# Kernel tuning notes

Hardware: AMD Instinct MI355X
Metric: run time of the kernel (lower is better)

Reference implementation:

```python
import jax, jax.numpy as jnp
import numpy as np

N, E, D, L = 10000, 160000, 512, 3
NEG_SLOPE = 0.2
LN_EPS = 1e-5


def setup_inputs() -> dict:
    key = jax.random.key(0)
    ks = jax.random.split(key, 16)
    def rn(k, shape, scale=0.02):
        return jax.random.normal(k, shape, dtype=jnp.float32) * scale
    return {
        "x": jax.random.normal(ks[0], (N, D), dtype=jnp.float32),
        "edge_attr": jax.random.normal(ks[1], (E, 2), dtype=jnp.float32),
        "emb_inv_W": rn(ks[2], (D, D)), "emb_inv_b": jnp.zeros((D,), jnp.float32),
        "emb_org_W": rn(ks[3], (D, D)), "emb_org_b": jnp.zeros((D,), jnp.float32),
        "gat_Wl": rn(ks[4], (L, D, D)), "gat_bl": jnp.zeros((L, D), jnp.float32),
        "gat_Wr": rn(ks[5], (L, D, D)), "gat_br": jnp.zeros((L, D), jnp.float32),
        "gat_We": rn(ks[6], (L, 2, D)),
        "gat_att": rn(ks[7], (L, D), 0.1),
        "gat_bias": jnp.zeros((L, D), jnp.float32),
        "ln_g": jnp.ones((L, D), jnp.float32), "ln_b": jnp.zeros((L, D), jnp.float32),
        "lin0_W": rn(ks[8], (2 * D, D)), "lin0_b": jnp.zeros((D,), jnp.float32),
        "lin1_W": rn(ks[9], (2 * D, D)), "lin1_b": jnp.zeros((D,), jnp.float32),
        "edge_index": jax.random.randint(ks[10], (2, E), 0, N, dtype=jnp.int32),
        "n_inv": 4000,
        "n_unknown": 3000,
    }


def _layernorm(x, g, b):
    m = jnp.mean(x, axis=-1, keepdims=True)
    v = jnp.mean((x - m) ** 2, axis=-1, keepdims=True)
    return (x - m) * jax.lax.rsqrt(v + LN_EPS) * g + b


def _gatv2(x, src, dst, edge_attr, Wl, bl, Wr, br, We, att, bias):
    # single-head GATv2: e_ij = att . leaky_relu(Wl x_j + Wr x_i + We e_ij)
    xl = x @ Wl + bl                                  # [N,D] source transform
    xr = x @ Wr + br                                  # [N,D] target transform
    m = xl[src] + xr[dst] + edge_attr @ We            # [E,D]
    s = jax.nn.leaky_relu(m, NEG_SLOPE) @ att         # [E] attention logits
    smax = jax.ops.segment_max(s, dst, num_segments=N)  # per-target max
    a = jnp.exp(s - smax[dst])
    denom = jax.ops.segment_sum(a, dst, num_segments=N)
    alpha = a / jnp.where(denom[dst] > 0, denom[dst], 1.0)  # [E]
    out = jax.ops.segment_sum(alpha[:, None] * xl[src], dst, num_segments=N)
    return out + bias


def _forward(x, edge_attr, emb_inv_W, emb_inv_b, emb_org_W, emb_org_b,
             gat_Wl, gat_bl, gat_Wr, gat_br, gat_We, gat_att, gat_bias,
             ln_g, ln_b, lin0_W, lin0_b, lin1_W, lin1_b,
             edge_index, n_inv, n_unknown):
    src, dst = edge_index[0], edge_index[1]
    x0 = x[:n_inv] @ emb_inv_W + emb_inv_b           # [n_inv, D]
    x1 = x[n_inv:] @ emb_org_W + emb_org_b           # [N-n_inv, D]
    h = jnp.concatenate([x0, x1], axis=0)            # [N, D]
    for k in range(L):
        hc = _gatv2(h, src, dst, edge_attr,
                    gat_Wl[k], gat_bl[k], gat_Wr[k], gat_br[k],
                    gat_We[k], gat_att[k], gat_bias[k])
        h = jax.nn.relu(_layernorm(hc + h, ln_g[k], ln_b[k]))
    y0 = jnp.concatenate([x0, h[:n_inv]], axis=-1) @ lin0_W + lin0_b          # [n_inv, D]
    y1 = jnp.concatenate([x1[-n_unknown:], h[-n_unknown:]], axis=-1) @ lin1_W + lin1_b  # [n_unknown, D]
    return y0 @ y1.T                                  # [n_inv, n_unknown]


def reference(x, edge_attr, emb_inv_W, emb_inv_b, emb_org_W, emb_org_b,
              gat_Wl, gat_bl, gat_Wr, gat_br, gat_We, gat_att, gat_bias,
              ln_g, ln_b, lin0_W, lin0_b, lin1_W, lin1_b,
              edge_index, n_inv, n_unknown):
    return _forward(x, edge_attr, emb_inv_W, emb_inv_b, emb_org_W, emb_org_b,
                    gat_Wl, gat_bl, gat_Wr, gat_br, gat_We, gat_att, gat_bias,
                    ln_g, ln_b, lin0_W, lin0_b, lin1_W, lin1_b,
                    edge_index, n_inv, n_unknown)
```

## Files before the change

kernel.cpp:

```cpp
#include <hip/hip_runtime.h>
#include <cstddef>
#include <cstdint>

namespace {

using u16 = unsigned short;
typedef __attribute__((ext_vector_type(8))) unsigned short u16x8;
typedef __attribute__((ext_vector_type(8))) short bf16x8;
typedef __attribute__((ext_vector_type(4))) float f32x4;

constexpr int kN    = 10000;
constexpr int kE    = 160000;
constexpr int kD    = 512;
constexpr int kNinv = 4000;
constexpr int kNunk = 3000;
constexpr int kND   = kN * kD;
constexpr float kLnEps = 1e-5f;

__device__ __forceinline__ float bf2f(u16 u) {
  return __uint_as_float((unsigned)u << 16);
}
__device__ __forceinline__ u16 f2bf(float f) {
  unsigned u = __float_as_uint(f);
  return (u16)((u + 0x7FFFu + ((u >> 16) & 1u)) >> 16);
}

__device__ __forceinline__ void gload_lds16(const void* g, void* l) {
  __builtin_amdgcn_global_load_lds(
      (const __attribute__((address_space(1))) void*)(unsigned long long)(uintptr_t)g,
      (__attribute__((address_space(3))) void*)(unsigned)(uintptr_t)l,
      16, 0, 0);
}

template <bool WRITE_F32, bool WRITE_BF16>
__global__ __launch_bounds__(256) void gemm_bf16(
    const u16* __restrict__ A1, const u16* __restrict__ A2,
    const u16* __restrict__ BT, const float* __restrict__ bias,
    float* __restrict__ Cf, u16* __restrict__ Cb, u16* __restrict__ Cb2,
    int nsplit, int M, int N, int K, int ldc) {
  __shared__ u16 As[128 * 64];
  __shared__ u16 Bs[128 * 64];
  const int tid  = threadIdx.x;
  const int lane = tid & 63;
  const int wid  = tid >> 6;

  const int nwg = gridDim.x * gridDim.y;
  int wg = blockIdx.x + gridDim.x * blockIdx.y;
  {
    const int xcd = wg & 7, idx = wg >> 3;
    const int q = nwg >> 3, r = nwg & 7;
    wg = (xcd < r ? xcd * (q + 1) : r * (q + 1) + (xcd - r) * q) + idx;
  }
  const int bm = (wg % gridDim.x) * 128;
  const int bn = (wg / gridDim.x) * 128;

  const int wr = (wid >> 1) * 64;
  const int wc = (wid & 1) * 64;

  f32x4 acc[4][4];
#pragma unroll
  for (int m = 0; m < 4; ++m)
#pragma unroll
    for (int n = 0; n < 4; ++n) acc[m][n] = (f32x4){0.f, 0.f, 0.f, 0.f};

  const int srow = lane >> 3;
  const int slot = lane & 7;
  const size_t astride = (A2 != nullptr) ? 512 : (size_t)K;

  for (int k0 = 0; k0 < K; k0 += 64) {
    const u16* Ap = A1;
    int kof = k0;
    if (A2 != nullptr && k0 >= 512) { Ap = A2; kof = k0 - 512; }
#pragma unroll
    for (int t = 0; t < 4; ++t) {
      const int inst = wid * 4 + t;
      const int row  = inst * 8 + srow;
      const int scol = ((slot ^ (row & 7)) << 4);
      const int ar   = min(bm + row, M - 1);
      gload_lds16((const char*)Ap + ((size_t)ar * astride + kof) * 2 + scol,
                  (char*)As + inst * 1024);
    }
#pragma unroll
    for (int t = 0; t < 4; ++t) {
      const int inst = wid * 4 + t;
      const int row  = inst * 8 + srow;
      const int scol = ((slot ^ (row & 7)) << 4);
      const int bc   = min(bn + row, N - 1);
      gload_lds16((const char*)BT + ((size_t)bc * K + k0) * 2 + scol,
                  (char*)Bs + inst * 1024);
    }
    asm volatile("s_waitcnt vmcnt(0)" ::: "memory");
    __syncthreads();

#pragma unroll
    for (int kk = 0; kk < 2; ++kk) {
      bf16x8 af[4], bfr[4];
#pragma unroll
      for (int m = 0; m < 4; ++m) {
        const int r = wr + m * 16 + (lane & 15);
        const int s = kk * 4 + (lane >> 4);
        af[m] = *(const bf16x8*)((const char*)As + r * 128 + ((s ^ (r & 7)) << 4));
      }
#pragma unroll
      for (int n = 0; n < 4; ++n) {
        const int c = wc + n * 16 + (lane & 15);
        const int s = kk * 4 + (lane >> 4);
        bfr[n] = *(const bf16x8*)((const char*)Bs + c * 128 + ((s ^ (c & 7)) << 4));
      }
#pragma unroll
      for (int m = 0; m < 4; ++m)
#pragma unroll
        for (int n = 0; n < 4; ++n)
          acc[m][n] = __builtin_amdgcn_mfma_f32_16x16x32_bf16(bfr[n], af[m],
                                                              acc[m][n], 0, 0, 0);
    }
    __syncthreads();
  }

#pragma unroll
  for (int m = 0; m < 4; ++m) {
    const int r = bm + wr + m * 16 + (lane & 15);
    if (r >= M) continue;
#pragma unroll
    for (int n = 0; n < 4; ++n) {
      const int c0 = bn + wc + n * 16 + ((lane >> 4) << 2);
      if (c0 >= N) continue;
      float4 bv = make_float4(0.f, 0.f, 0.f, 0.f);
      if (bias != nullptr) bv = *reinterpret_cast<const float4*>(bias + c0);
      float v0 = acc[m][n][0] + bv.x;
      float v1 = acc[m][n][1] + bv.y;
      float v2 = acc[m][n][2] + bv.z;
      float v3 = acc[m][n][3] + bv.w;
      if (WRITE_F32) {
        float4 o; o.x = v0; o.y = v1; o.z = v2; o.w = v3;
        *reinterpret_cast<float4*>(Cf + (size_t)r * ldc + c0) = o;
      }
      if (WRITE_BF16) {
        u16* dstp = Cb;
        int c = c0;
        if (Cb2 != nullptr && c0 >= nsplit) { dstp = Cb2; c = c0 - nsplit; }
        ushort4 o;
        o.x = f2bf(v0); o.y = f2bf(v1); o.z = f2bf(v2); o.w = f2bf(v3);
        *reinterpret_cast<ushort4*>(dstp + (size_t)r * ldc + c) = o;
      }
    }
  }
}

__global__ __launch_bounds__(256) void gat_fused_kernel(
    const u16* __restrict__ xl, const u16* __restrict__ xr,
    const int* __restrict__ esrcS, const float2* __restrict__ eaS,
    const int* __restrict__ offs, const float* __restrict__ We,
    const float* __restrict__ att, const float* __restrict__ bias,
    const float* __restrict__ lng, const float* __restrict__ lnb,
    const u16* __restrict__ resid, u16* __restrict__ hb) {
  __shared__ float accLDS[4][512];
  __shared__ float wsLDS[4];
  const int wid = threadIdx.x >> 6, lane = threadIdx.x & 63;
  const int n = blockIdx.x;
  const int d8 = lane * 8;

  float r8[8], w0[8], w1[8], a06[8], a04[8];
  {
    const u16x8 rv = *(const u16x8*)(xr + (size_t)n * kD + d8);
#pragma unroll
    for (int i = 0; i < 8; ++i) {
      r8[i] = bf2f(rv[i]);
      w0[i] = We[d8 + i];
      w1[i] = We[kD + d8 + i];
      const float a = att[d8 + i];
      a06[i] = 0.6f * a;
      a04[i] = 0.4f * a;
    }
  }

  float acc[8];
#pragma unroll
  for (int j = 0; j < 8; ++j) acc[j] = 0.f;
  float l_run = 0.f;

  const int beg = offs[n], end = offs[n + 1];
  const int cnt = end - beg;
  const int q = cnt >> 2, r = cnt & 3;
  const int myCnt = q + ((wid < r) ? 1 : 0);
  const int myBeg = beg + wid * q + min(wid, r);

  int sv = 0;
  float2 e2 = make_float2(0.f, 0.f);
  if (lane < myCnt) {
    sv = esrcS[myBeg + lane];
    e2 = eaS[myBeg + lane];
  }

  for (int i = 0; i < myCnt; i += 4) {
    const int k = myCnt - i;
    u16x8 rows[4];
#pragma unroll
    for (int t = 0; t < 4; ++t)
      if (t < k)
        rows[t] = *(const u16x8*)(xl + (size_t)__shfl(sv, i + t) * kD + d8);
    float s[4];
#pragma unroll
    for (int t = 0; t < 4; ++t) {
      s[t] = 0.f;
      if (t < k) {
        const float ex = __shfl(e2.x, i + t), ey = __shfl(e2.y, i + t);
#pragma unroll
        for (int j = 0; j < 8; ++j) {
          const float m = bf2f(rows[t][j]) + r8[j] + ex * w0[j] + ey * w1[j];
          s[t] += a06[j] * m + a04[j] * fabsf(m);
        }
      }
    }
#pragma unroll
    for (int off = 32; off > 0; off >>= 1)
#pragma unroll
      for (int t = 0; t < 4; ++t)
        if (t < k) s[t] += __shfl_xor(s[t], off);
    float qv[4];
    float ws = 0.f;
#pragma unroll
    for (int t = 0; t < 4; ++t) {
      qv[t] = (t < k) ? __expf(s[t]) : 0.f;
      ws += qv[t];
    }
    l_run += ws;
#pragma unroll
    for (int j = 0; j < 8; ++j) {
      float v = acc[j];
#pragma unroll
      for (int t = 0; t < 4; ++t)
        if (t < k) v += qv[t] * bf2f(rows[t][j]);
      acc[j] = v;
    }
  }

  if (lane == 0) wsLDS[wid] = l_run;
#pragma unroll
  for (int j = 0; j < 8; ++j) accLDS[wid][j * 64 + lane] = acc[j];
  __syncthreads();

  if (wid == 0) {
    const float l = wsLDS[0] + wsLDS[1] + wsLDS[2] + wsLDS[3];
    const float inv = 1.f / (l > 0.f ? l : 1.f);
    float aT[8];
#pragma unroll
    for (int j = 0; j < 8; ++j)
      aT[j] = accLDS[0][j * 64 + lane] + accLDS[1][j * 64 + lane] +
              accLDS[2][j * 64 + lane] + accLDS[3][j * 64 + lane];

    float xv[8];
    float sum = 0.f, sq = 0.f;
    {
      const u16x8 hv8 = *(const u16x8*)(resid + (size_t)n * kD + d8);
#pragma unroll
      for (int j = 0; j < 8; ++j) {
        xv[j] = bf2f(hv8[j]) + aT[j] * inv + bias[d8 + j];
        sum += xv[j];
        sq  += xv[j] * xv[j];
      }
    }
#pragma unroll
    for (int off = 32; off > 0; off >>= 1) {
      sum += __shfl_xor(sum, off);
      sq  += __shfl_xor(sq, off);
    }
    const float mean = sum * (1.f / kD);
    const float var  = sq * (1.f / kD) - mean * mean;
    const float rs = rsqrtf(var + kLnEps);
    u16x8 pk;
#pragma unroll
    for (int j = 0; j < 8; ++j) {
      const float y = fmaxf((xv[j] - mean) * rs * lng[d8 + j] + lnb[d8 + j], 0.f);
      pk[j] = f2bf(y);
    }
    *(u16x8*)(hb + (size_t)n * kD + d8) = pk;
  }
}

struct TxJobs {
  const float* src[10];
  u16* dst[10];
  int K[10];
};

__global__ __launch_bounds__(256) void transpose_all_kernel(TxJobs jobs) {
  const int z = blockIdx.z;
  const int K = jobs.K[z];
  const int k0 = blockIdx.x * 32;
  if (k0 >= K) return;
  const int n0 = blockIdx.y * 32;
  const float* W = jobs.src[z];
  u16* WT = jobs.dst[z];
  __shared__ float t[32][33];
  const int lx = threadIdx.x & 31, ly = threadIdx.x >> 5;
#pragma unroll
  for (int r = 0; r < 32; r += 8)
    t[ly + r][lx] = W[(size_t)(k0 + ly + r) * 512 + n0 + lx];
  __syncthreads();
#pragma unroll
  for (int r = 0; r < 32; r += 8)
    WT[(size_t)(n0 + ly + r) * K + k0 + lx] = f2bf(t[lx][ly + r]);
}

__global__ void convert_bf16_kernel(const float* __restrict__ in,
                                    u16* __restrict__ out, int n4) {
  const int i = blockIdx.x * 256 + threadIdx.x;
  if (i >= n4) return;
  const float4 v = reinterpret_cast<const float4*>(in)[i];
  u16 o[4] = {f2bf(v.x), f2bf(v.y), f2bf(v.z), f2bf(v.w)};
  *reinterpret_cast<ulonglong1*>(out + (size_t)i * 4) =
      *reinterpret_cast<ulonglong1*>(o);
}

__global__ void catbias_kernel(const float* __restrict__ bl,
                               const float* __restrict__ br,
                               float* __restrict__ catB) {
  const int i = blockIdx.x * 256 + threadIdx.x;
  if (i >= 3 * 1024) return;
  const int k = i >> 10, j = i & 1023;
  catB[i] = (j < 512) ? bl[k * 512 + j] : br[k * 512 + j - 512];
}

__global__ void fill_i32(int* p, int v, int n) {
  const int i = blockIdx.x * 256 + threadIdx.x;
  if (i < n) p[i] = v;
}
__global__ void copy_i32(const int* a, int* b, int n) {
  const int i = blockIdx.x * 256 + threadIdx.x;
  if (i < n) b[i] = a[i];
}
__global__ void count_kernel(const int* __restrict__ dst, int* __restrict__ counts) {
  const int e = blockIdx.x * 256 + threadIdx.x;
  if (e < kE) atomicAdd(&counts[dst[e]], 1);
}
__global__ __launch_bounds__(1024) void scan_kernel(const int* __restrict__ counts,
                                                    int* __restrict__ offs, int n) {
  __shared__ int buf[1024];
  __shared__ int carry;
  const int tid = threadIdx.x;
  if (tid == 0) carry = 0;
  __syncthreads();
  for (int base = 0; base < n; base += 1024) {
    const int v = (base + tid < n) ? counts[base + tid] : 0;
    buf[tid] = v;
    __syncthreads();
    for (int off = 1; off < 1024; off <<= 1) {
      const int t = (tid >= off) ? buf[tid - off] : 0;
      __syncthreads();
      buf[tid] += t;
      __syncthreads();
    }
    if (base + tid < n) offs[base + tid] = carry + buf[tid] - v;
    __syncthreads();
    if (tid == 0) carry += buf[1023];
    __syncthreads();
  }
  if (tid == 0) offs[n] = carry;
}
__global__ void scatter_kernel(const int* __restrict__ dst,
                               const int* __restrict__ src,
                               const float* __restrict__ ea,
                               int* __restrict__ pos,
                               int* __restrict__ esrcS,
                               float2* __restrict__ eaS) {
  const int e = blockIdx.x * 256 + threadIdx.x;
  if (e >= kE) return;
  const int p = atomicAdd(&pos[dst[e]], 1);
  esrcS[p] = src[e];
  eaS[p] = *(const float2*)(ea + (size_t)e * 2);
}

}

extern "C" void kernel_launch(void* const* d_in, const int* in_sizes, int n_in,
                              void* d_out, int out_size, void* d_ws, size_t ws_size,
                              hipStream_t stream) {
  const float* x         = (const float*)d_in[0];
  const float* edge_attr = (const float*)d_in[1];
  const float* emb_inv_W = (const float*)d_in[2];
  const float* emb_inv_b = (const float*)d_in[3];
  const float* emb_org_W = (const float*)d_in[4];
  const float* emb_org_b = (const float*)d_in[5];
  const float* gat_Wl    = (const float*)d_in[6];
  const float* gat_bl    = (const float*)d_in[7];
  const float* gat_Wr    = (const float*)d_in[8];
  const float* gat_br    = (const float*)d_in[9];
  const float* gat_We    = (const float*)d_in[10];
  const float* gat_att   = (const float*)d_in[11];
  const float* gat_bias  = (const float*)d_in[12];
  const float* ln_g      = (const float*)d_in[13];
  const float* ln_b      = (const float*)d_in[14];
  const float* lin0_W    = (const float*)d_in[15];
  const float* lin0_b    = (const float*)d_in[16];
  const float* lin1_W    = (const float*)d_in[17];
  const float* lin1_b    = (const float*)d_in[18];
  const int*   edge_idx  = (const int*)d_in[19];
  const int* src = edge_idx;
  const int* dst = edge_idx + kE;
  float* out = (float*)d_out;

  float* catB = (float*)d_ws;
  u16* xb   = (u16*)(catB + 3072);
  u16* hb0  = xb + kND;
  u16* hb   = hb0 + kND;
  u16* xlB  = hb + kND;
  u16* xrB  = xlB + kND;
  u16* y0b  = xrB + kND;
  u16* y1b  = y0b + kNinv * kD;
  u16* embInvT = y1b + kNunk * kD;
  u16* embOrgT = embInvT + 262144;
  u16* WlrT    = embOrgT + 262144;
  u16* lin0T   = WlrT + 3 * 524288;
  u16* lin1T   = lin0T + 524288;
  int* counts  = (int*)(lin1T + 524288);
  int* offs    = counts + kN;
  int* pos     = offs + kN + 1;
  int* esrcS   = pos + kN;
  float2* eaS  = (float2*)(esrcS + kE);

  const dim3 blk(256);
  auto cdiv = [](int a, int b) { return (a + b - 1) / b; };

  {
    TxJobs j;
    j.src[0] = emb_inv_W;  j.dst[0] = embInvT;  j.K[0] = 512;
    j.src[1] = emb_org_W;  j.dst[1] = embOrgT;  j.K[1] = 512;
    for (int k = 0; k < 3; ++k) {
      j.src[2 + k] = gat_Wl + (size_t)k * kD * kD;
      j.dst[2 + k] = WlrT + (size_t)k * 524288;
      j.K[2 + k] = 512;
      j.src[5 + k] = gat_Wr + (size_t)k * kD * kD;
      j.dst[5 + k] = WlrT + (size_t)k * 524288 + 262144;
      j.K[5 + k] = 512;
    }
    j.src[8] = lin0_W; j.dst[8] = lin0T; j.K[8] = 1024;
    j.src[9] = lin1_W; j.dst[9] = lin1T; j.K[9] = 1024;
    transpose_all_kernel<<<dim3(32, 16, 10), blk, 0, stream>>>(j);
  }
  convert_bf16_kernel<<<dim3(cdiv(kND / 4, 256)), blk, 0, stream>>>(x, xb, kND / 4);
  catbias_kernel<<<dim3(12), blk, 0, stream>>>(gat_bl, gat_br, catB);

  gemm_bf16<false, true><<<dim3(cdiv(kNinv, 128), 4), blk, 0, stream>>>(
      xb, nullptr, embInvT, emb_inv_b, nullptr, hb0, nullptr, 0, kNinv, kD, kD, kD);
  gemm_bf16<false, true><<<dim3(cdiv(kN - kNinv, 128), 4), blk, 0, stream>>>(
      xb + (size_t)kNinv * kD, nullptr, embOrgT, emb_org_b,
      nullptr, hb0 + (size_t)kNinv * kD, nullptr, 0, kN - kNinv, kD, kD, kD);

  fill_i32<<<dim3(cdiv(kN, 256)), blk, 0, stream>>>(counts, 0, kN);
  count_kernel<<<dim3(cdiv(kE, 256)), blk, 0, stream>>>(dst, counts);
  scan_kernel<<<dim3(1), dim3(1024), 0, stream>>>(counts, offs, kN);
  copy_i32<<<dim3(cdiv(kN, 256)), blk, 0, stream>>>(offs, pos, kN);
  scatter_kernel<<<dim3(cdiv(kE, 256)), blk, 0, stream>>>(dst, src, edge_attr, pos,
                                                          esrcS, eaS);

  for (int k = 0; k < 3; ++k) {
    const u16* hIn = (k == 0) ? hb0 : hb;
    gemm_bf16<false, true><<<dim3(cdiv(kN, 128), 8), blk, 0, stream>>>(
        hIn, nullptr, WlrT + (size_t)k * 524288, catB + k * 1024,
        nullptr, xlB, xrB, 512, kN, 1024, kD, kD);
    gat_fused_kernel<<<dim3(kN), blk, 0, stream>>>(
        xlB, xrB, esrcS, eaS, offs,
        gat_We + (size_t)k * 2 * kD, gat_att + (size_t)k * kD,
        gat_bias + (size_t)k * kD, ln_g + (size_t)k * kD,
        ln_b + (size_t)k * kD, hIn, hb);
  }

  gemm_bf16<false, true><<<dim3(cdiv(kNinv, 128), 4), blk, 0, stream>>>(
      hb0, hb, lin0T, lin0_b, nullptr, y0b, nullptr, 0, kNinv, kD, 2 * kD, kD);
  const size_t off = (size_t)(kN - kNunk) * kD;
  gemm_bf16<false, true><<<dim3(cdiv(kNunk, 128), 4), blk, 0, stream>>>(
      hb0 + off, hb + off, lin1T, lin1_b, nullptr, y1b, nullptr, 0,
      kNunk, kD, 2 * kD, kD);

  gemm_bf16<true, false><<<dim3(cdiv(kNinv, 128), cdiv(kNunk, 128)), blk, 0, stream>>>(
      y0b, nullptr, y1b, nullptr, out, nullptr, nullptr, 0,
      kNinv, kNunk, kD, kNunk);
}
```

Measured before the change: 413.7 us.

## Process four nodes per GAT block and spread LayerNorm epilogue across all waves

The fused GAT kernel now loops over four destination nodes per block instead of one. This cuts the grid size and reuses the per-thread We/att register loads across nodes. The LayerNorm/residual epilogue, which previously ran only on wave 0, is now split across all 256 threads with two elements each, using a cross-wave LDS reduction for mean and variance. The cost is extra __syncthreads per node, serialization of four nodes within a block, and less latency hiding from having fewer blocks.

```diff
diff --git a/kernel.cpp b/kernel.cpp
--- a/kernel.cpp
+++ b/kernel.cpp
@@ -15,6 +15,7 @@
 constexpr int kNinv = 4000;
 constexpr int kNunk = 3000;
 constexpr int kND   = kN * kD;
+constexpr int kNodesPerBlk = 4;
 constexpr float kLnEps = 1e-5f;
 
 __device__ __forceinline__ float bf2f(u16 u) {
@@ -156,125 +157,126 @@
     const u16* __restrict__ resid, u16* __restrict__ hb) {
   __shared__ float accLDS[4][512];
   __shared__ float wsLDS[4];
+  __shared__ float red_s[4], red_q[4];
   const int wid = threadIdx.x >> 6, lane = threadIdx.x & 63;
-  const int n = blockIdx.x;
   const int d8 = lane * 8;
 
-  float r8[8], w0[8], w1[8], a06[8], a04[8];
-  {
-    const u16x8 rv = *(const u16x8*)(xr + (size_t)n * kD + d8);
-#pragma unroll
-    for (int i = 0; i < 8; ++i) {
-      r8[i] = bf2f(rv[i]);
-      w0[i] = We[d8 + i];
-      w1[i] = We[kD + d8 + i];
-      const float a = att[d8 + i];
-      a06[i] = 0.6f * a;
-      a04[i] = 0.4f * a;
-    }
-  }
-
-  float acc[8];
-#pragma unroll
-  for (int j = 0; j < 8; ++j) acc[j] = 0.f;
-  float l_run = 0.f;
-
-  const int beg = offs[n], end = offs[n + 1];
-  const int cnt = end - beg;
-  const int q = cnt >> 2, r = cnt & 3;
-  const int myCnt = q + ((wid < r) ? 1 : 0);
-  const int myBeg = beg + wid * q + min(wid, r);
-
-  int sv = 0;
-  float2 e2 = make_float2(0.f, 0.f);
-  if (lane < myCnt) {
-    sv = esrcS[myBeg + lane];
-    e2 = eaS[myBeg + lane];
-  }
-
-  for (int i = 0; i < myCnt; i += 4) {
-    const int k = myCnt - i;
-    u16x8 rows[4];
-#pragma unroll
-    for (int t = 0; t < 4; ++t)
-      if (t < k)
-        rows[t] = *(const u16x8*)(xl + (size_t)__shfl(sv, i + t) * kD + d8);
-    float s[4];
-#pragma unroll
-    for (int t = 0; t < 4; ++t) {
-      s[t] = 0.f;
-      if (t < k) {
-        const float ex = __shfl(e2.x, i + t), ey = __shfl(e2.y, i + t);
-#pragma unroll
-        for (int j = 0; j < 8; ++j) {
-          const float m = bf2f(rows[t][j]) + r8[j] + ex * w0[j] + ey * w1[j];
-          s[t] += a06[j] * m + a04[j] * fabsf(m);
+  float w0[8], w1[8], a06[8], a04[8];
+#pragma unroll
+  for (int i = 0; i < 8; ++i) {
+    w0[i] = We[d8 + i];
+    w1[i] = We[kD + d8 + i];
+    const float a = att[d8 + i];
+    a06[i] = 0.6f * a;
+    a04[i] = 0.4f * a;
+  }
+
+  const int nBase = blockIdx.x * kNodesPerBlk;
+  for (int nn = 0; nn < kNodesPerBlk; ++nn) {
+    const int n = nBase + nn;
+    if (n >= kN) break;
+
+    float r8[8];
+    {
+      const u16x8 rv = *(const u16x8*)(xr + (size_t)n * kD + d8);
+#pragma unroll
+      for (int i = 0; i < 8; ++i) r8[i] = bf2f(rv[i]);
+    }
+
+    float acc[8];
+#pragma unroll
+    for (int j = 0; j < 8; ++j) acc[j] = 0.f;
+    float l_run = 0.f;
+
+    const int beg = offs[n], end = offs[n + 1];
+    const int cnt = end - beg;
+    const int q = cnt >> 2, r = cnt & 3;
+    const int myCnt = q + ((wid < r) ? 1 : 0);
+    const int myBeg = beg + wid * q + min(wid, r);
+
+    int sv = 0;
+    float2 e2 = make_float2(0.f, 0.f);
+    if (lane < myCnt) {
+      sv = esrcS[myBeg + lane];
+      e2 = eaS[myBeg + lane];
+    }
+
+    for (int i = 0; i < myCnt; i += 4) {
+      const int k = myCnt - i;
+      u16x8 rows[4];
+#pragma unroll
+      for (int t = 0; t < 4; ++t)
+        if (t < k)
+          rows[t] = *(const u16x8*)(xl + (size_t)__shfl(sv, i + t) * kD + d8);
+      float s[4];
+#pragma unroll
+      for (int t = 0; t < 4; ++t) {
+        s[t] = 0.f;
+        if (t < k) {
+          const float ex = __shfl(e2.x, i + t), ey = __shfl(e2.y, i + t);
+#pragma unroll
+          for (int j = 0; j < 8; ++j) {
+            const float m = bf2f(rows[t][j]) + r8[j] + ex * w0[j] + ey * w1[j];
+            s[t] += a06[j] * m + a04[j] * fabsf(m);
+          }
         }
       }
-    }
-#pragma unroll
-    for (int off = 32; off > 0; off >>= 1)
-#pragma unroll
-      for (int t = 0; t < 4; ++t)
-        if (t < k) s[t] += __shfl_xor(s[t], off);
-    float qv[4];
-    float ws = 0.f;
-#pragma unroll
-    for (int t = 0; t < 4; ++t) {
-      qv[t] = (t < k) ? __expf(s[t]) : 0.f;
-      ws += qv[t];
-    }
-    l_run += ws;
-#pragma unroll
-    for (int j = 0; j < 8; ++j) {
-      float v = acc[j];
-#pragma unroll
-      for (int t = 0; t < 4; ++t)
-        if (t < k) v += qv[t] * bf2f(rows[t][j]);
-      acc[j] = v;
-    }
-  }
-
-  if (lane == 0) wsLDS[wid] = l_run;
-#pragma unroll
-  for (int j = 0; j < 8; ++j) accLDS[wid][j * 64 + lane] = acc[j];
-  __syncthreads();
-
-  if (wid == 0) {
+#pragma unroll
+      for (int off = 32; off > 0; off >>= 1)
+#pragma unroll
+        for (int t = 0; t < 4; ++t)
+          if (t < k) s[t] += __shfl_xor(s[t], off);
+      float qv[4];
+      float ws = 0.f;
+#pragma unroll
+      for (int t = 0; t < 4; ++t) {
+        qv[t] = (t < k) ? __expf(s[t]) : 0.f;
+        ws += qv[t];
+      }
+      l_run += ws;
+#pragma unroll
+      for (int j = 0; j < 8; ++j) {
+        float v = acc[j];
+#pragma unroll
+        for (int t = 0; t < 4; ++t)
+          if (t < k) v += qv[t] * bf2f(rows[t][j]);
+        acc[j] = v;
+      }
+    }
+
+    if (lane == 0) wsLDS[wid] = l_run;
+#pragma unroll
+    for (int j = 0; j < 8; ++j) accLDS[wid][j * 64 + lane] = acc[j];
+    __syncthreads();
+
+    const int d2 = threadIdx.x * 2;
+    const int i0 = ((d2 & 7) << 6) + (d2 >> 3);
+    const int i1 = (((d2 + 1) & 7) << 6) + (d2 >> 3);
     const float l = wsLDS[0] + wsLDS[1] + wsLDS[2] + wsLDS[3];
     const float inv = 1.f / (l > 0.f ? l : 1.f);
-    float aT[8];
-#pragma unroll
-    for (int j = 0; j < 8; ++j)
-      aT[j] = accLDS[0][j * 64 + lane] + accLDS[1][j * 64 + lane] +
-              accLDS[2][j * 64 + lane] + accLDS[3][j * 64 + lane];
-
-    float xv[8];
-    float sum = 0.f, sq = 0.f;
-    {
-      const u16x8 hv8 = *(const u16x8*)(resid + (size_t)n * kD + d8);
-#pragma unroll
-      for (int j = 0; j < 8; ++j) {
-        xv[j] = bf2f(hv8[j]) + aT[j] * inv + bias[d8 + j];
-        sum += xv[j];
-        sq  += xv[j] * xv[j];
-      }
-    }
+    const float a0 = accLDS[0][i0] + accLDS[1][i0] + accLDS[2][i0] + accLDS[3][i0];
+    const float a1 = accLDS[0][i1] + accLDS[1][i1] + accLDS[2][i1] + accLDS[3][i1];
+    const unsigned hv = *(const unsigned*)(resid + (size_t)n * kD + d2);
+    const float x0 = __uint_as_float(hv << 16)         + a0 * inv + bias[d2];
+    const float x1 = __uint_as_float(hv & 0xffff0000u) + a1 * inv + bias[d2 + 1];
+    float sum = x0 + x1, sq = x0 * x0 + x1 * x1;
 #pragma unroll
     for (int off = 32; off > 0; off >>= 1) {
       sum += __shfl_xor(sum, off);
       sq  += __shfl_xor(sq, off);
     }
+    if (lane == 0) { red_s[wid] = sum; red_q[wid] = sq; }
+    __syncthreads();
+    sum = red_s[0] + red_s[1] + red_s[2] + red_s[3];
+    sq  = red_q[0] + red_q[1] + red_q[2] + red_q[3];
     const float mean = sum * (1.f / kD);
     const float var  = sq * (1.f / kD) - mean * mean;
     const float rs = rsqrtf(var + kLnEps);
-    u16x8 pk;
-#pragma unroll
-    for (int j = 0; j < 8; ++j) {
-      const float y = fmaxf((xv[j] - mean) * rs * lng[d8 + j] + lnb[d8 + j], 0.f);
-      pk[j] = f2bf(y);
-    }
-    *(u16x8*)(hb + (size_t)n * kD + d8) = pk;
+    const float y0 = fmaxf((x0 - mean) * rs * lng[d2]     + lnb[d2],     0.f);
+    const float y1 = fmaxf((x1 - mean) * rs * lng[d2 + 1] + lnb[d2 + 1], 0.f);
+    const unsigned packed = (unsigned)f2bf(y0) | ((unsigned)f2bf(y1) << 16);
+    *(unsigned*)(hb + (size_t)n * kD + d2) = packed;
+    __syncthreads();
   }
 }
 
@@ -459,7 +461,7 @@
     gemm_bf16<false, true><<<dim3(cdiv(kN, 128), 8), blk, 0, stream>>>(
         hIn, nullptr, WlrT + (size_t)k * 524288, catB + k * 1024,
         nullptr, xlB, xrB, 512, kN, 1024, kD, kD);
-    gat_fused_kernel<<<dim3(kN), blk, 0, stream>>>(
+    gat_fused_kernel<<<dim3(cdiv(kN, kNodesPerBlk)), blk, 0, stream>>>(
         xlB, xrB, esrcS, eaS, offs,
         gat_We + (size_t)k * 2 * kD, gat_att + (size_t)k * kD,
         gat_bias + (size_t)k * kD, ln_g + (size_t)k * kD,
```

Result: slower. 475.8 us (+15.0%).

## Assign one wavefront per destination node in GAT kernel and fold pos copy into scan

Applied to the files above, without the earlier changes.

The fused GAT aggregation kernel now gives each wavefront its own target node (four nodes per block) instead of splitting one node's edges across four wavefronts. This removes the LDS reduction, the __syncthreads, and the idle three wavefronts during the LayerNorm epilogue. Edges are processed in chunks of 64 per wavefront. Separately, the scan kernel writes the offsets into pos directly, which drops the copy_i32 launch. The trade-off is less parallelism for nodes with high degree, and load imbalance between wavefronts in the same block.

```diff
diff --git a/kernel.cpp b/kernel.cpp
--- a/kernel.cpp
+++ b/kernel.cpp
@@ -154,10 +154,9 @@
     const float* __restrict__ att, const float* __restrict__ bias,
     const float* __restrict__ lng, const float* __restrict__ lnb,
     const u16* __restrict__ resid, u16* __restrict__ hb) {
-  __shared__ float accLDS[4][512];
-  __shared__ float wsLDS[4];
   const int wid = threadIdx.x >> 6, lane = threadIdx.x & 63;
-  const int n = blockIdx.x;
+  const int n = blockIdx.x * 4 + wid;
+  if (n >= kN) return;
   const int d8 = lane * 8;
 
   float r8[8], w0[8], w1[8], a06[8], a04[8];
@@ -180,102 +179,84 @@
   float l_run = 0.f;
 
   const int beg = offs[n], end = offs[n + 1];
-  const int cnt = end - beg;
-  const int q = cnt >> 2, r = cnt & 3;
-  const int myCnt = q + ((wid < r) ? 1 : 0);
-  const int myBeg = beg + wid * q + min(wid, r);
-
-  int sv = 0;
-  float2 e2 = make_float2(0.f, 0.f);
-  if (lane < myCnt) {
-    sv = esrcS[myBeg + lane];
-    e2 = eaS[myBeg + lane];
-  }
-
-  for (int i = 0; i < myCnt; i += 4) {
-    const int k = myCnt - i;
-    u16x8 rows[4];
-#pragma unroll
-    for (int t = 0; t < 4; ++t)
-      if (t < k)
-        rows[t] = *(const u16x8*)(xl + (size_t)__shfl(sv, i + t) * kD + d8);
-    float s[4];
-#pragma unroll
-    for (int t = 0; t < 4; ++t) {
-      s[t] = 0.f;
-      if (t < k) {
-        const float ex = __shfl(e2.x, i + t), ey = __shfl(e2.y, i + t);
-#pragma unroll
-        for (int j = 0; j < 8; ++j) {
-          const float m = bf2f(rows[t][j]) + r8[j] + ex * w0[j] + ey * w1[j];
-          s[t] += a06[j] * m + a04[j] * fabsf(m);
+  for (int base = beg; base < end; base += 64) {
+    const int cnt = min(64, end - base);
+    const int idx = base + ((lane < cnt) ? lane : 0);
+    const int sv = esrcS[idx];
+    const float2 e2 = eaS[idx];
+
+    for (int i = 0; i < cnt; i += 4) {
+      const int k = cnt - i;
+      u16x8 rows[4];
+#pragma unroll
+      for (int t = 0; t < 4; ++t)
+        if (t < k)
+          rows[t] = *(const u16x8*)(xl + (size_t)__shfl(sv, i + t) * kD + d8);
+      float s[4];
+#pragma unroll
+      for (int t = 0; t < 4; ++t) {
+        s[t] = 0.f;
+        if (t < k) {
+          const float ex = __shfl(e2.x, i + t), ey = __shfl(e2.y, i + t);
+#pragma unroll
+          for (int j = 0; j < 8; ++j) {
+            const float m = bf2f(rows[t][j]) + r8[j] + ex * w0[j] + ey * w1[j];
+            s[t] += a06[j] * m + a04[j] * fabsf(m);
+          }
         }
       }
-    }
-#pragma unroll
-    for (int off = 32; off > 0; off >>= 1)
-#pragma unroll
-      for (int t = 0; t < 4; ++t)
-        if (t < k) s[t] += __shfl_xor(s[t], off);
-    float qv[4];
-    float ws = 0.f;
-#pragma unroll
-    for (int t = 0; t < 4; ++t) {
-      qv[t] = (t < k) ? __expf(s[t]) : 0.f;
-      ws += qv[t];
-    }
-    l_run += ws;
+#pragma unroll
+      for (int off = 32; off > 0; off >>= 1)
+#pragma unroll
+        for (int t = 0; t < 4; ++t)
+          if (t < k) s[t] += __shfl_xor(s[t], off);
+      float qv[4];
+      float ws = 0.f;
+#pragma unroll
+      for (int t = 0; t < 4; ++t) {
+        qv[t] = (t < k) ? __expf(s[t]) : 0.f;
+        ws += qv[t];
+      }
+      l_run += ws;
+#pragma unroll
+      for (int j = 0; j < 8; ++j) {
+        float v = acc[j];
+#pragma unroll
+        for (int t = 0; t < 4; ++t)
+          if (t < k) v += qv[t] * bf2f(rows[t][j]);
+        acc[j] = v;
+      }
+    }
+  }
+
+  const float inv = 1.f / (l_run > 0.f ? l_run : 1.f);
+
+  float xv[8];
+  float sum = 0.f, sq = 0.f;
+  {
+    const u16x8 hv8 = *(const u16x8*)(resid + (size_t)n * kD + d8);
 #pragma unroll
     for (int j = 0; j < 8; ++j) {
-      float v = acc[j];
-#pragma unroll
-      for (int t = 0; t < 4; ++t)
-        if (t < k) v += qv[t] * bf2f(rows[t][j]);
-      acc[j] = v;
-    }
-  }
-
-  if (lane == 0) wsLDS[wid] = l_run;
-#pragma unroll
-  for (int j = 0; j < 8; ++j) accLDS[wid][j * 64 + lane] = acc[j];
-  __syncthreads();
-
-  if (wid == 0) {
-    const float l = wsLDS[0] + wsLDS[1] + wsLDS[2] + wsLDS[3];
-    const float inv = 1.f / (l > 0.f ? l : 1.f);
-    float aT[8];
-#pragma unroll
-    for (int j = 0; j < 8; ++j)
-      aT[j] = accLDS[0][j * 64 + lane] + accLDS[1][j * 64 + lane] +
-              accLDS[2][j * 64 + lane] + accLDS[3][j * 64 + lane];
-
-    float xv[8];
-    float sum = 0.f, sq = 0.f;
-    {
-      const u16x8 hv8 = *(const u16x8*)(resid + (size_t)n * kD + d8);
-#pragma unroll
-      for (int j = 0; j < 8; ++j) {
-        xv[j] = bf2f(hv8[j]) + aT[j] * inv + bias[d8 + j];
-        sum += xv[j];
-        sq  += xv[j] * xv[j];
-      }
-    }
-#pragma unroll
-    for (int off = 32; off > 0; off >>= 1) {
-      sum += __shfl_xor(sum, off);
-      sq  += __shfl_xor(sq, off);
-    }
-    const float mean = sum * (1.f / kD);
-    const float var  = sq * (1.f / kD) - mean * mean;
-    const float rs = rsqrtf(var + kLnEps);
-    u16x8 pk;
-#pragma unroll
-    for (int j = 0; j < 8; ++j) {
-      const float y = fmaxf((xv[j] - mean) * rs * lng[d8 + j] + lnb[d8 + j], 0.f);
-      pk[j] = f2bf(y);
-    }
-    *(u16x8*)(hb + (size_t)n * kD + d8) = pk;
-  }
+      xv[j] = bf2f(hv8[j]) + acc[j] * inv + bias[d8 + j];
+      sum += xv[j];
+      sq  += xv[j] * xv[j];
+    }
+  }
+#pragma unroll
+  for (int off = 32; off > 0; off >>= 1) {
+    sum += __shfl_xor(sum, off);
+    sq  += __shfl_xor(sq, off);
+  }
+  const float mean = sum * (1.f / kD);
+  const float var  = sq * (1.f / kD) - mean * mean;
+  const float rs = rsqrtf(var + kLnEps);
+  u16x8 pk;
+#pragma unroll
+  for (int j = 0; j < 8; ++j) {
+    const float y = fmaxf((xv[j] - mean) * rs * lng[d8 + j] + lnb[d8 + j], 0.f);
+    pk[j] = f2bf(y);
+  }
+  *(u16x8*)(hb + (size_t)n * kD + d8) = pk;
 }
 
 struct TxJobs {
@@ -326,16 +307,13 @@
   const int i = blockIdx.x * 256 + threadIdx.x;
   if (i < n) p[i] = v;
 }
-__global__ void copy_i32(const int* a, int* b, int n) {
-  const int i = blockIdx.x * 256 + threadIdx.x;
-  if (i < n) b[i] = a[i];
-}
 __global__ void count_kernel(const int* __restrict__ dst, int* __restrict__ counts) {
   const int e = blockIdx.x * 256 + threadIdx.x;
   if (e < kE) atomicAdd(&counts[dst[e]], 1);
 }
 __global__ __launch_bounds__(1024) void scan_kernel(const int* __restrict__ counts,
-                                                    int* __restrict__ offs, int n) {
+                                                    int* __restrict__ offs,
+                                                    int* __restrict__ pos, int n) {
   __shared__ int buf[1024];
   __shared__ int carry;
   const int tid = threadIdx.x;
@@ -351,7 +329,11 @@
       buf[tid] += t;
       __syncthreads();
     }
-    if (base + tid < n) offs[base + tid] = carry + buf[tid] - v;
+    if (base + tid < n) {
+      const int ex = carry + buf[tid] - v;
+      offs[base + tid] = ex;
+      pos[base + tid] = ex;
+    }
     __syncthreads();
     if (tid == 0) carry += buf[1023];
     __syncthreads();
@@ -449,8 +431,7 @@
 
   fill_i32<<<dim3(cdiv(kN, 256)), blk, 0, stream>>>(counts, 0, kN);
   count_kernel<<<dim3(cdiv(kE, 256)), blk, 0, stream>>>(dst, counts);
-  scan_kernel<<<dim3(1), dim3(1024), 0, stream>>>(counts, offs, kN);
-  copy_i32<<<dim3(cdiv(kN, 256)), blk, 0, stream>>>(offs, pos, kN);
+  scan_kernel<<<dim3(1), dim3(1024), 0, stream>>>(counts, offs, pos, kN);
   scatter_kernel<<<dim3(cdiv(kE, 256)), blk, 0, stream>>>(dst, src, edge_attr, pos,
                                                           esrcS, eaS);
 
@@ -459,7 +440,7 @@
     gemm_bf16<false, true><<<dim3(cdiv(kN, 128), 8), blk, 0, stream>>>(
         hIn, nullptr, WlrT + (size_t)k * 524288, catB + k * 1024,
         nullptr, xlB, xrB, 512, kN, 1024, kD, kD);
-    gat_fused_kernel<<<dim3(kN), blk, 0, stream>>>(
+    gat_fused_kernel<<<dim3(cdiv(kN, 4)), blk, 0, stream>>>(
         xlB, xrB, esrcS, eaS, offs,
         gat_We + (size_t)k * 2 * kD, gat_att + (size_t)k * kD,
         gat_bias + (size_t)k * kD, ln_g + (size_t)k * kD,
```

After: 424.2 us. 1.03x slower.
